# Kernel optimization log

Measured on AMD Instinct MI355X. Metric: run time of the kernel, lower is better.

## Reference

```python
import jax, jax.numpy as jnp
import numpy as np

B, T = 32768, 32
OBJ_V, PRED_V = 179, 46
E_OBJ, E_PRED, H = 5, 5, 32
IN_DIM = E_OBJ + E_PRED + 2 + 4  # 16, matches LSTMCell input size


def setup_inputs() -> dict:
    key = jax.random.key(0)
    ks = jax.random.split(key, 12)
    s = 0.1
    return {
        "input_objects": jax.random.randint(ks[0], (B, T), 0, OBJ_V),
        "input_boxes": jax.random.uniform(ks[1], (B, T, 4), dtype=jnp.float32),
        "predicates": jax.random.randint(ks[2], (B, T), 0, PRED_V),
        "subject_indicators": jax.random.randint(ks[3], (B, T), 0, 2),
        "target_object": jax.random.randint(ks[4], (B,), 0, OBJ_V),
        "obj_emb": jax.random.normal(ks[5], (OBJ_V, E_OBJ), dtype=jnp.float32) * s,
        "pred_emb": jax.random.normal(ks[6], (PRED_V, E_PRED), dtype=jnp.float32) * s,
        "W_ih": jax.random.normal(ks[7], (4 * H, IN_DIM), dtype=jnp.float32) * s,
        "W_hh": jax.random.normal(ks[8], (4 * H, H), dtype=jnp.float32) * s,
        "b_ih": jnp.zeros((4 * H,), dtype=jnp.float32),
        "b_hh": jnp.zeros((4 * H,), dtype=jnp.float32),
        "fc2_W": jax.random.normal(ks[9], (4, H), dtype=jnp.float32) * s,
        "fc2_b": jnp.zeros((4,), dtype=jnp.float32),
    }


def _forward(input_objects, input_boxes, predicates, subject_indicators,
             obj_emb, pred_emb, W_ih, W_hh, b_ih, b_hh, fc2_W, fc2_b):
    # concatenate_features, vectorized over all timesteps at once: [B,T,16]
    feats = jnp.concatenate([
        obj_emb[input_objects],                                   # [B,T,5]
        pred_emb[predicates],                                     # [B,T,5]
        jax.nn.one_hot(subject_indicators, 2, dtype=jnp.float32), # [B,T,2]
        input_boxes,                                              # [B,T,4]
    ], axis=-1)
    xs = jnp.transpose(feats, (1, 0, 2))  # [T,B,16] for scan over time

    def step(carry, x):
        h, c = carry
        gates = x @ W_ih.T + b_ih + h @ W_hh.T + b_hh  # [B,4H]
        i, f, g, o = jnp.split(gates, 4, axis=-1)      # torch gate order i,f,g,o
        i = jax.nn.sigmoid(i)
        f = jax.nn.sigmoid(f)
        g = jnp.tanh(g)
        o = jax.nn.sigmoid(o)
        c = f * c + i * g
        h = o * jnp.tanh(c)
        return (h, c), None

    h0 = jnp.zeros((input_objects.shape[0], H), dtype=jnp.float32)
    (h, _), _ = jax.lax.scan(step, (h0, h0), xs)
    out = h @ fc2_W.T + fc2_b          # output_fc2 on last hidden state
    return jnp.clip(out, 0.0, 1.0)     # torch.clamp(min=0, max=1)


def reference(input_objects, input_boxes, predicates, subject_indicators, target_object,
              obj_emb, pred_emb, W_ih, W_hh, b_ih, b_hh, fc2_W, fc2_b):
    # target_object is accepted by the torch forward but unused in its body
    return _forward(input_objects, input_boxes, predicates, subject_indicators,
                    obj_emb, pred_emb, W_ih, W_hh, b_ih, b_hh, fc2_W, fc2_b)
```

## Files before the change

### kernel.cpp

```cpp
#include <hip/hip_runtime.h>

#define LDS_BYTES 18720

typedef _Float16 f16x8 __attribute__((ext_vector_type(8)));
typedef float    f32x4 __attribute__((ext_vector_type(4)));

#define LOG2E     1.44269504088896f
#define TWO_LOG2E 2.88539008177793f

__device__ __forceinline__ float sig_pre(float a) {
    return __builtin_amdgcn_rcpf(1.0f + __builtin_amdgcn_exp2f(a));
}
__device__ __forceinline__ float tanh_pre(float a) {
    return 1.0f - 2.0f * __builtin_amdgcn_rcpf(1.0f + __builtin_amdgcn_exp2f(a));
}
__device__ __forceinline__ int pack2(float a, float b) {
    union { _Float16 h[2]; int i; } u;
    u.h[0] = (_Float16)a; u.h[1] = (_Float16)b;
    return u.i;
}

__global__ __launch_bounds__(256, 8)
void lstm_fused(const int* __restrict__ objs,
                const float* __restrict__ boxes,
                const int* __restrict__ preds,
                const int* __restrict__ subj,
                const float* __restrict__ obj_emb,
                const float* __restrict__ pred_emb,
                const float* __restrict__ W_ih,
                const float* __restrict__ W_hh,
                const float* __restrict__ b_ih,
                const float* __restrict__ b_hh,
                const float* __restrict__ fc2_W,
                const float* __restrict__ fc2_b,
                float* __restrict__ out)
{
    extern __shared__ char smem[];
    const int tid  = threadIdx.x;
    const int lane = tid & 63;
    const int wv   = tid >> 6;
    const int quad = lane >> 4;
    const int cidx = lane & 15;
    const int XOFF = 0, HX0 = 16640, HX1 = 17664, ZOFF = 18688;

    if (tid < 8) ((int*)(smem + ZOFF))[tid] = 0;

    {
        int b  = tid >> 4;
        int t0 = (tid & 15) << 1;
        long gb = (long)blockIdx.x * 16 + b;
        int2 ov = *(const int2*)(objs  + gb * 32 + t0);
        int2 pv = *(const int2*)(preds + gb * 32 + t0);
        int2 sv = *(const int2*)(subj  + gb * 32 + t0);
        int oarr[2] = {ov.x, ov.y};
        int parr[2] = {pv.x, pv.y};
        int sarr[2] = {sv.x, sv.y};
        #pragma unroll
        for (int tt = 0; tt < 2; ++tt) {
            int t = t0 + tt;
            const float* eo = obj_emb  + oarr[tt] * 5;
            const float* ep = pred_emb + parr[tt] * 5;
            float4 bx = *(const float4*)(boxes + (gb * 32 + t) * 4);
            f16x8 lo, hi;
            lo[0]=(_Float16)eo[0]; lo[1]=(_Float16)eo[1]; lo[2]=(_Float16)eo[2];
            lo[3]=(_Float16)eo[3]; lo[4]=(_Float16)eo[4];
            lo[5]=(_Float16)ep[0]; lo[6]=(_Float16)ep[1]; lo[7]=(_Float16)ep[2];
            hi[0]=(_Float16)ep[3]; hi[1]=(_Float16)ep[4];
            hi[2]=(_Float16)(sarr[tt]==0 ? 1.0f : 0.0f);
            hi[3]=(_Float16)(sarr[tt]==1 ? 1.0f : 0.0f);
            hi[4]=(_Float16)bx.x; hi[5]=(_Float16)bx.y;
            hi[6]=(_Float16)bx.z; hi[7]=(_Float16)bx.w;
            char* dst = smem + XOFF + b * 1040 + t * 32;
            *(f16x8*)dst        = lo;
            *(f16x8*)(dst + 16) = hi;
        }
    }

    f16x8 Wf[2][2];
    f32x4 bias4[2];
    #pragma unroll
    for (int tile = 0; tile < 2; ++tile) {
        int rm   = cidx & 3;
        int u    = 8 * (cidx >> 2) + 2 * wv + (rm & 1);
        int gate = tile * 2 + (rm >> 1);
        float scale = (gate == 2) ? TWO_LOG2E : -LOG2E;
        int n = gate * 32 + u;
        #pragma unroll
        for (int ks = 0; ks < 2; ++ks) {
            f16x8 v;
            #pragma unroll
            for (int jj = 0; jj < 8; ++jj) {
                int k = ks * 32 + quad * 8 + jj;
                float val = (k < 16) ? W_ih[n * 16 + k]
                          : (k >= 32) ? W_hh[n * 32 + (k - 32)]
                          : 0.0f;
                v[jj] = (_Float16)(val * scale);
            }
            Wf[tile][ks] = v;
        }
        #pragma unroll
        for (int r = 0; r < 4; ++r) {
            int ur = 8 * quad + 2 * wv + (r & 1);
            int gr = tile * 2 + (r >> 1);
            float sc = (gr == 2) ? TWO_LOG2E : -LOG2E;
            bias4[tile][r] = (b_ih[gr * 32 + ur] + b_hh[gr * 32 + ur]) * sc;
        }
    }

    const bool qlow = (quad < 2);
    int       xaddr = qlow ? (XOFF + cidx * 1040 + quad * 16) : ZOFF;
    const int xinc  = qlow ? 32 : 0;
    const int slot  = lane * 4;

    __syncthreads();

    f16x8 xfrag = *(const f16x8*)(smem + xaddr); xaddr += xinc;
    f32x4 accp[2];
    #pragma unroll
    for (int tile = 0; tile < 2; ++tile)
        accp[tile] = __builtin_amdgcn_mfma_f32_16x16x32_f16(Wf[tile][0], xfrag, bias4[tile], 0, 0, 0);

    union { int i[4]; f16x8 v; } hf;
    hf.i[0] = 0; hf.i[1] = 0; hf.i[2] = 0; hf.i[3] = 0;
    float cst[2] = {0, 0};
    float h0, h1;

    #pragma unroll 2
    for (int t = 0; t < 32; ++t) {
        f32x4 acc0 = __builtin_amdgcn_mfma_f32_16x16x32_f16(Wf[0][1], hf.v, accp[0], 0, 0, 0);
        f32x4 acc1 = __builtin_amdgcn_mfma_f32_16x16x32_f16(Wf[1][1], hf.v, accp[1], 0, 0, 0);

        f16x8 xn = *(const f16x8*)(smem + xaddr); xaddr += xinc;

        float i0 = sig_pre(acc0[0]);
        float i1 = sig_pre(acc0[1]);
        float f0 = sig_pre(acc0[2]);
        float f1 = sig_pre(acc0[3]);
        float g0 = tanh_pre(acc1[0]);
        float g1 = tanh_pre(acc1[1]);
        float o0 = sig_pre(acc1[2]);
        float o1 = sig_pre(acc1[3]);
        float c0 = fmaf(f0, cst[0], i0 * g0);
        float c1 = fmaf(f1, cst[1], i1 * g1);
        cst[0] = c0; cst[1] = c1;
        h0 = o0 * tanh_pre(c0 * TWO_LOG2E);
        h1 = o1 * tanh_pre(c1 * TWO_LOG2E);
        int pk = pack2(h0, h1);

        char* buf = smem + ((t & 1) ? HX1 : HX0);
        *(int*)(buf + wv * 256 + slot) = pk;

        accp[0] = __builtin_amdgcn_mfma_f32_16x16x32_f16(Wf[0][0], xn, bias4[0], 0, 0, 0);
        accp[1] = __builtin_amdgcn_mfma_f32_16x16x32_f16(Wf[1][0], xn, bias4[1], 0, 0, 0);

        __syncthreads();
        hf.i[0] = *(const int*)(buf + 0   + slot);
        hf.i[1] = *(const int*)(buf + 256 + slot);
        hf.i[2] = *(const int*)(buf + 512 + slot);
        hf.i[3] = *(const int*)(buf + 768 + slot);
    }

    __syncthreads();
    {
        int u0 = 8 * quad + 2 * wv;
        *(float2*)(smem + cidx * 144 + u0 * 4) = (float2){h0, h1};
    }
    __syncthreads();

    if (tid < 64) {
        int b = tid >> 2, jj = tid & 3;
        const float* fw   = fc2_W + jj * 32;
        const float* hrow = (const float*)(smem + b * 144);
        float s = fc2_b[jj];
        #pragma unroll
        for (int k = 0; k < 8; ++k) {
            float4 hv = *(const float4*)(hrow + k * 4);
            s += fw[k*4+0] * hv.x + fw[k*4+1] * hv.y
               + fw[k*4+2] * hv.z + fw[k*4+3] * hv.w;
        }
        s = fminf(fmaxf(s, 0.0f), 1.0f);
        out[(long)blockIdx.x * 64 + tid] = s;
    }
}

extern "C" void kernel_launch(void* const* d_in, const int* in_sizes, int n_in,
                              void* d_out, int out_size, void* d_ws, size_t ws_size,
                              hipStream_t stream)
{
    lstm_fused<<<2048, 256, LDS_BYTES, stream>>>(
        (const int*)d_in[0], (const float*)d_in[1], (const int*)d_in[2],
        (const int*)d_in[3],
        (const float*)d_in[5], (const float*)d_in[6],
        (const float*)d_in[7], (const float*)d_in[8],
        (const float*)d_in[9], (const float*)d_in[10],
        (const float*)d_in[11], (const float*)d_in[12],
        (float*)d_out);
}
```

Before: 138.3 us.

## Fold LSTM gate divisions into fewer reciprocals and stagger block start times

Each step of the cell update is rewritten algebraically. The sigmoid and tanh divisions for c are merged into one combined fraction, and those for h into another, so each step needs two reciprocals per unit instead of five while keeping the same exp2 count. A per-block s_sleep delay before the first barrier spreads out workgroups that would otherwise run in lockstep on the transcendental and MFMA units. The combined products can overflow to inf and give NaN for large pre-activations, and the sleep adds up to a few microseconds of idle time per block.

```diff
diff --git a/kernel.cpp b/kernel.cpp
--- a/kernel.cpp
+++ b/kernel.cpp
@@ -8,12 +8,6 @@
 #define LOG2E     1.44269504088896f
 #define TWO_LOG2E 2.88539008177793f
 
-__device__ __forceinline__ float sig_pre(float a) {
-    return __builtin_amdgcn_rcpf(1.0f + __builtin_amdgcn_exp2f(a));
-}
-__device__ __forceinline__ float tanh_pre(float a) {
-    return 1.0f - 2.0f * __builtin_amdgcn_rcpf(1.0f + __builtin_amdgcn_exp2f(a));
-}
 __device__ __forceinline__ int pack2(float a, float b) {
     union { _Float16 h[2]; int i; } u;
     u.h[0] = (_Float16)a; u.h[1] = (_Float16)b;
@@ -112,6 +106,11 @@
     const int xinc  = qlow ? 32 : 0;
     const int slot  = lane * 4;
 
+    {
+        int del = (blockIdx.x * 37) & 31;
+        while (del--) asm volatile("s_sleep 2" ::: "memory");
+    }
+
     __syncthreads();
 
     f16x8 xfrag = *(const f16x8*)(smem + xaddr); xaddr += xinc;
@@ -132,19 +131,34 @@
 
         f16x8 xn = *(const f16x8*)(smem + xaddr); xaddr += xinc;
 
-        float i0 = sig_pre(acc0[0]);
-        float i1 = sig_pre(acc0[1]);
-        float f0 = sig_pre(acc0[2]);
-        float f1 = sig_pre(acc0[3]);
-        float g0 = tanh_pre(acc1[0]);
-        float g1 = tanh_pre(acc1[1]);
-        float o0 = sig_pre(acc1[2]);
-        float o1 = sig_pre(acc1[3]);
-        float c0 = fmaf(f0, cst[0], i0 * g0);
-        float c1 = fmaf(f1, cst[1], i1 * g1);
+        float Ei0 = __builtin_amdgcn_exp2f(acc0[0]);
+        float Ei1 = __builtin_amdgcn_exp2f(acc0[1]);
+        float Ef0 = __builtin_amdgcn_exp2f(acc0[2]);
+        float Ef1 = __builtin_amdgcn_exp2f(acc0[3]);
+        float Eg0 = __builtin_amdgcn_exp2f(acc1[0]);
+        float Eg1 = __builtin_amdgcn_exp2f(acc1[1]);
+        float Eo0 = __builtin_amdgcn_exp2f(acc1[2]);
+        float Eo1 = __builtin_amdgcn_exp2f(acc1[3]);
+
+        float t10  = 1.0f + Ei0;
+        float t11  = 1.0f + Ei1;
+        float dig0 = fmaf(t10, Eg0, t10);
+        float dig1 = fmaf(t11, Eg1, t11);
+        float tf0  = 1.0f + Ef0;
+        float tf1  = 1.0f + Ef1;
+        float n0   = fmaf(Eg0 - 1.0f, tf0, cst[0] * dig0);
+        float n1   = fmaf(Eg1 - 1.0f, tf1, cst[1] * dig1);
+        float c0   = n0 * __builtin_amdgcn_rcpf(tf0 * dig0);
+        float c1   = n1 * __builtin_amdgcn_rcpf(tf1 * dig1);
         cst[0] = c0; cst[1] = c1;
-        h0 = o0 * tanh_pre(c0 * TWO_LOG2E);
-        h1 = o1 * tanh_pre(c1 * TWO_LOG2E);
+        float Ec0  = __builtin_amdgcn_exp2f(c0 * TWO_LOG2E);
+        float Ec1  = __builtin_amdgcn_exp2f(c1 * TWO_LOG2E);
+        float to0  = 1.0f + Eo0;
+        float to1  = 1.0f + Eo1;
+        float dh0  = fmaf(to0, Ec0, to0);
+        float dh1  = fmaf(to1, Ec1, to1);
+        h0 = (Ec0 - 1.0f) * __builtin_amdgcn_rcpf(dh0);
+        h1 = (Ec1 - 1.0f) * __builtin_amdgcn_rcpf(dh1);
         int pk = pack2(h0, h1);
 
         char* buf = smem + ((t & 1) ? HX1 : HX0);
```

Result: faster. 133.7 us (-3.4%).
